# Kernel optimization log

Hardware: AMD Instinct MI355X
Metric: run time of the kernel (lower is better)

## Reference

```python
import jax, jax.numpy as jnp
import numpy as np

# ---- module hyperparameters (init_kwargs) ----
QMIN, QMAX, QBINS = -8.0, 8.0, 128
PMIN, PMAX, PBINS = -10.0, 10.0, 128
GAMMA_F = 1.0
N_TRAJ = 16384


def _grid():
    # x = arange(qmin - 4/gamma_f, qmax + 4/gamma_f + 0.1/maxp, 0.1/maxp)
    maxp = max(abs(PMIN), abs(PMAX))
    step = 0.1 / maxp
    x = np.arange(QMIN - 4.0 / GAMMA_F, QMAX + 4.0 / GAMMA_F + step, step)
    return x.astype(np.float32)


def setup_inputs() -> dict:
    key = jax.random.key(0)
    ks = jax.random.split(key, 6)
    shape = (1, N_TRAJ)
    x = jnp.asarray(_grid())
    # psi buffer: stand-in for np.interp(x, spl.x, spl.psis[-1][1]) -- a
    # localized oscillatory wavefunction sampled on the grid.
    psi = (jnp.exp(-0.5 * (x - 1.0) ** 2) * jnp.cos(2.0 * x)).astype(jnp.float32)
    return {
        "factors_re": jax.random.normal(ks[0], shape, jnp.float32),
        "factors_im": jax.random.normal(ks[1], shape, jnp.float32),
        "q_re": jax.random.normal(ks[2], shape, jnp.float32),
        "q_im": 0.5 * jax.random.normal(ks[3], shape, jnp.float32),
        "p_re": jax.random.normal(ks[4], shape, jnp.float32),
        "p_im": 0.5 * jax.random.normal(ks[5], shape, jnp.float32),
        "x": x,
        "psi": psi,
    }


def _trapz0(y, x):
    # trapezoid rule along axis 0; y: [M, N] (complex), x: [M]
    dx = jnp.diff(x)
    return jnp.sum(0.5 * (y[1:] + y[:-1]) * dx[:, None], axis=0)


def _forward(factors_re, factors_im, q_re, q_im, p_re, p_im, x, psi):
    g = GAMMA_F
    factors = factors_re + 1j * factors_im  # [1, N] complex
    # _calc_proj: xi = 2*g*q + 1j*p ; qf = Re(xi)/(2g), pf = Im(xi)
    qf = q_re - p_im / (2.0 * g)
    pf = 2.0 * g * q_im + p_re
    dq = (QMAX - QMIN) / QBINS
    dp = (PMAX - PMIN) / PBINS
    qb = jnp.floor((qf - QMIN) / dq)
    pb = jnp.floor((pf - PMIN) / dp)
    bins = (qb * PBINS + pb).astype(jnp.int32).reshape(-1)  # [N]
    n = bins.shape[0]
    # torch: enumerate(torch.unique(bins)) -> rank among sorted unique values.
    # jnp.unique inverse (size=n, large fill pads at the end) gives the same map.
    _, inv = jnp.unique(bins, return_inverse=True, size=n, fill_value=jnp.int32(2**30))
    inds = inv.reshape(qf.shape)  # [1, N] compact bin ids
    qc = (qb + 0.5) * dq + QMIN  # bin centers [1, N]
    pc = (pb + 0.5) * dp + PMIN
    # _gf: coherent-state Gaussians on grid x -> [M, N]
    norm = (2.0 * g / jnp.pi) ** 0.25
    dxq = x[:, None] - qc.reshape(-1)[None, :]  # [M, N]
    gfs = norm * jnp.exp(-g * dxq * dxq + 1j * pc.reshape(-1)[None, :] * dxq)
    gt = _trapz0(jnp.conj(gfs) * psi[:, None], x)  # [N] complex
    # _calc_pref (reconstruction): exponential prefactor that can blow up,
    # hence the nan_to_num + clamp in the original.
    pref = norm * jnp.exp(g * q_im * q_im + 1j * (p_re * q_im))  # [1, N]
    pref = (jnp.clip(jnp.nan_to_num(pref.real), -100.0, 100.0)
            + 1j * jnp.clip(jnp.nan_to_num(pref.imag), -100.0, 100.0))
    vals = pref * factors  # [1, N]
    b = vals.shape[0]
    binned = jnp.zeros_like(vals).at[jnp.arange(b)[:, None], inds].add(vals)
    loss = jnp.sum(jnp.abs(binned - gt[None, :]) ** 2)
    return jnp.sqrt(loss)


def reference(factors_re, factors_im, q_re, q_im, p_re, p_im, x, psi):
    return _forward(factors_re, factors_im, q_re, q_im, p_re, p_im, x, psi)
```

## Files before the change

### kernel.cpp

```cpp
#include <hip/hip_runtime.h>
#include <math.h>


#define PRES_WORDS 1024
#define PRES_BITS  65536
#define PRES_OFF   32768
#define CHUNKS     16
#define WINR       4.5f

__global__ void prep_kernel(const float* __restrict__ f_re, const float* __restrict__ f_im,
                            const float* __restrict__ q_re, const float* __restrict__ q_im,
                            const float* __restrict__ p_re, const float* __restrict__ p_im,
                            const float* __restrict__ x, const float* __restrict__ psi,
                            float* __restrict__ qc, float* __restrict__ pc,
                            float* __restrict__ vre, float* __restrict__ vim,
                            int* __restrict__ bins, unsigned long long* __restrict__ pres,
                            float* __restrict__ bre, float* __restrict__ bim,
                            float2* __restrict__ xw, int n, int M)
{
    int i = blockIdx.x * blockDim.x + threadIdx.x;
    if (i >= n) return;
    bre[i] = 0.0f; bim[i] = 0.0f;
    if (i < M) {
        float w;
        if (i == 0)          w = 0.5f * (x[1] - x[0]);
        else if (i == M - 1) w = 0.5f * (x[M - 1] - x[M - 2]);
        else                 w = 0.5f * (x[i + 1] - x[i - 1]);
        xw[i] = make_float2(x[i], w * psi[i] * 0.8932438417380023f);
    }
    const float norm = 0.8932438417380023f;
    float qi = q_im[i], pr = p_re[i];
    float qf = q_re[i] - 0.5f * p_im[i];
    float pf = 2.0f * qi + pr;
    float qb = floorf((qf - (-8.0f)) / 0.125f);
    float pb = floorf((pf - (-10.0f)) / 0.15625f);
    int b = (int)(qb * 128.0f + pb);
    bins[i] = b;
    int pidx = min(max(b + PRES_OFF, 0), PRES_BITS - 1);
    atomicOr(&pres[pidx >> 6], 1ull << (pidx & 63));
    qc[i] = (qb + 0.5f) * 0.125f + (-8.0f);
    pc[i] = (pb + 0.5f) * 0.15625f + (-10.0f);
    float ea = norm * expf(qi * qi);
    float s, c;
    __sincosf(pr * qi, &s, &c);
    float prr = fminf(fmaxf(ea * c, -100.0f), 100.0f);
    float pri = fminf(fmaxf(ea * s, -100.0f), 100.0f);
    float fr = f_re[i], fi = f_im[i];
    vre[i] = prr * fr - pri * fi;
    vim[i] = prr * fi + pri * fr;
}

__global__ void scatter_kernel(const int* __restrict__ bins,
                               const unsigned long long* __restrict__ pres,
                               const float* __restrict__ vre, const float* __restrict__ vim,
                               float* __restrict__ bre, float* __restrict__ bim, int n)
{
    __shared__ int lbase[PRES_WORDS];
    int tid = threadIdx.x;
    if (tid < 64) {
        int cum[16];
        int tot = 0;
        for (int k = 0; k < 16; k++) {
            cum[k] = tot;
            tot += __popcll(pres[tid * 16 + k]);
        }
        int run = tot;
        for (int off = 1; off < 64; off <<= 1) {
            int up = __shfl_up(run, off);
            if (tid >= off) run += up;
        }
        int excl = run - tot;
        for (int k = 0; k < 16; k++) lbase[tid * 16 + k] = excl + cum[k];
    }
    __syncthreads();
    int i = blockIdx.x * blockDim.x + tid;
    if (i >= n) return;
    int pidx = min(max(bins[i] + PRES_OFF, 0), PRES_BITS - 1);
    int w = pidx >> 6, bit = pidx & 63;
    unsigned long long below = pres[w] & ((bit == 0) ? 0ull : (~0ull >> (64 - bit)));
    int cid = lbase[w] + __popcll(below);
    atomicAdd(&bre[cid], vre[i]);
    atomicAdd(&bim[cid], vim[i]);
}

__global__ void gt_kernel(const float2* __restrict__ xw, const float* __restrict__ x,
                          const float* __restrict__ qc, const float* __restrict__ pc,
                          float* __restrict__ gpre, float* __restrict__ gpim,
                          int n, int M)
{
    int t = blockIdx.x * blockDim.x + threadIdx.x;
    if (t >= n) return;
    float qcn = qc[t], pcn = pc[t];
    float x0f = x[0];
    float flo = (qcn - WINR - x0f) * 100.0f;
    float fhi = (qcn + WINR - x0f) * 100.0f;
    int mlo = max(0, (int)flo - 1);
    int mhi = min(M, (int)fhi + 2);
    int len = mhi - mlo; if (len < 0) len = 0;
    int c = blockIdx.y;
    int ms = mlo + (len * c) / CHUNKS;
    int me = mlo + (len * (c + 1)) / CHUNKS;
    float sre = 0.0f, sim = 0.0f;
    for (int m = ms; m < me; m++) {
        float2 xm = xw[m];
        float dxq = xm.x - qcn;
        float e = __expf(-dxq * dxq) * xm.y;
        float s, cc;
        __sincosf(pcn * dxq, &s, &cc);
        sre = fmaf(e, cc, sre);
        sim = fmaf(-e, s, sim);
    }
    gpre[c * n + t] = sre;
    gpim[c * n + t] = sim;
}

__global__ void loss_final_kernel(const float* __restrict__ gpre, const float* __restrict__ gpim,
                                  const float* __restrict__ bre, const float* __restrict__ bim,
                                  float* __restrict__ loss, int* __restrict__ donecnt,
                                  float* __restrict__ out, int n)
{
    int t = blockIdx.x * blockDim.x + threadIdx.x;
    float v = 0.0f;
    if (t < n) {
        float sre = 0.0f, sim = 0.0f;
        for (int c = 0; c < CHUNKS; c++) {
            sre += gpre[c * n + t];
            sim += gpim[c * n + t];
        }
        float dre = bre[t] - sre;
        float dim = bim[t] - sim;
        v = dre * dre + dim * dim;
    }
#pragma unroll
    for (int off = 32; off > 0; off >>= 1) v += __shfl_down(v, off);
    __shared__ float l[4];
    int wv = threadIdx.x >> 6, ln = threadIdx.x & 63;
    if (ln == 0) l[wv] = v;
    __syncthreads();
    if (threadIdx.x == 0) {
        atomicAdd(loss, l[0] + l[1] + l[2] + l[3]);
        __threadfence();
        int old = atomicAdd(donecnt, 1);
        if (old == (int)gridDim.x - 1) {
            __threadfence();
            out[0] = sqrtf(atomicAdd(loss, 0.0f));
        }
    }
}

extern "C" void kernel_launch(void* const* d_in, const int* in_sizes, int n_in,
                              void* d_out, int out_size, void* d_ws, size_t ws_size,
                              hipStream_t stream)
{
    const float* f_re = (const float*)d_in[0];
    const float* f_im = (const float*)d_in[1];
    const float* q_re = (const float*)d_in[2];
    const float* q_im = (const float*)d_in[3];
    const float* p_re = (const float*)d_in[4];
    const float* p_im = (const float*)d_in[5];
    const float* x    = (const float*)d_in[6];
    const float* psi  = (const float*)d_in[7];
    int n = in_sizes[0];
    int M = in_sizes[6];

    float* wsf  = (float*)d_ws;
    float* qc   = wsf;
    float* pc   = qc + n;
    float* vre  = pc + n;
    float* vim  = vre + n;
    int*   bins = (int*)(vim + n);
    float* bre  = (float*)(bins + n);
    float* bim  = bre + n;
    float* gpre = bim + n;
    float* gpim = gpre + (size_t)CHUNKS * n;
    float2* xw  = (float2*)(gpim + (size_t)CHUNKS * n);
    unsigned long long* pres = (unsigned long long*)(xw + 4096);
    float* loss = (float*)(pres + PRES_WORDS);
    int*   donecnt = (int*)(loss + 1);

    hipMemsetAsync(pres, 0, PRES_WORDS * sizeof(unsigned long long) + 8, stream);

    int nb = (n + 255) / 256;
    prep_kernel<<<nb, 256, 0, stream>>>(f_re, f_im, q_re, q_im, p_re, p_im, x, psi,
                                        qc, pc, vre, vim, bins, pres, bre, bim, xw, n, M);
    scatter_kernel<<<nb, 256, 0, stream>>>(bins, pres, vre, vim, bre, bim, n);
    gt_kernel<<<dim3(nb, CHUNKS), 256, 0, stream>>>(xw, x, qc, pc, gpre, gpim, n, M);
    loss_final_kernel<<<nb, 256, 0, stream>>>(gpre, gpim, bre, bim, loss, donecnt,
                                              (float*)d_out, n);
}
```

Measured before the change: 118.1 us.

## Fuse scatter into Gaussian projection kernel and stage grid weights in shared memory

Merges the scatter-add kernel into the chunked Gaussian overlap kernel, so only the y=0 blocks perform the bin-rank computation and atomic adds. This removes one kernel launch. The grid/weight table is copied into LDS once per block instead of being read from global memory in the inner loop. The chunk count drops from 16 to 8 and the Gaussian truncation window shrinks from 4.5 to 4.0, which cuts per-thread loop work but adds slightly more tail-truncation error and assumes M fits in MCAP.

```diff
diff --git a/kernel.cpp b/kernel.cpp
--- a/kernel.cpp
+++ b/kernel.cpp
@@ -5,8 +5,9 @@
 #define PRES_WORDS 1024
 #define PRES_BITS  65536
 #define PRES_OFF   32768
-#define CHUNKS     16
-#define WINR       4.5f
+#define CHUNKS     8
+#define MCAP       2432
+#define WINR       4.0f
 
 __global__ void prep_kernel(const float* __restrict__ f_re, const float* __restrict__ f_im,
                             const float* __restrict__ q_re, const float* __restrict__ q_im,
@@ -50,20 +51,22 @@
     vim[i] = prr * fi + pri * fr;
 }
 
-__global__ void scatter_kernel(const int* __restrict__ bins,
-                               const unsigned long long* __restrict__ pres,
-                               const float* __restrict__ vre, const float* __restrict__ vim,
-                               float* __restrict__ bre, float* __restrict__ bim, int n)
+__global__ void __launch_bounds__(256) gt_scatter_kernel(
+    const float2* __restrict__ xw, const float* __restrict__ x,
+    const float* __restrict__ qc, const float* __restrict__ pc,
+    const int* __restrict__ bins, const unsigned long long* __restrict__ pres,
+    const float* __restrict__ vre, const float* __restrict__ vim,
+    float* __restrict__ bre, float* __restrict__ bim,
+    float* __restrict__ gpre, float* __restrict__ gpim, int n, int M)
 {
+    __shared__ float2 sxw[MCAP];
     __shared__ int lbase[PRES_WORDS];
     int tid = threadIdx.x;
-    if (tid < 64) {
+    for (int m = tid; m < M; m += 256) sxw[m] = xw[m];
+    if (blockIdx.y == 0 && tid < 64) {
         int cum[16];
         int tot = 0;
-        for (int k = 0; k < 16; k++) {
-            cum[k] = tot;
-            tot += __popcll(pres[tid * 16 + k]);
-        }
+        for (int k = 0; k < 16; k++) { cum[k] = tot; tot += __popcll(pres[tid * 16 + k]); }
         int run = tot;
         for (int off = 1; off < 64; off <<= 1) {
             int up = __shfl_up(run, off);
@@ -73,23 +76,16 @@
         for (int k = 0; k < 16; k++) lbase[tid * 16 + k] = excl + cum[k];
     }
     __syncthreads();
-    int i = blockIdx.x * blockDim.x + tid;
-    if (i >= n) return;
-    int pidx = min(max(bins[i] + PRES_OFF, 0), PRES_BITS - 1);
-    int w = pidx >> 6, bit = pidx & 63;
-    unsigned long long below = pres[w] & ((bit == 0) ? 0ull : (~0ull >> (64 - bit)));
-    int cid = lbase[w] + __popcll(below);
-    atomicAdd(&bre[cid], vre[i]);
-    atomicAdd(&bim[cid], vim[i]);
-}
-
-__global__ void gt_kernel(const float2* __restrict__ xw, const float* __restrict__ x,
-                          const float* __restrict__ qc, const float* __restrict__ pc,
-                          float* __restrict__ gpre, float* __restrict__ gpim,
-                          int n, int M)
-{
-    int t = blockIdx.x * blockDim.x + threadIdx.x;
+    int t = blockIdx.x * 256 + tid;
     if (t >= n) return;
+    if (blockIdx.y == 0) {
+        int pidx = min(max(bins[t] + PRES_OFF, 0), PRES_BITS - 1);
+        int w = pidx >> 6, bit = pidx & 63;
+        unsigned long long below = pres[w] & ((bit == 0) ? 0ull : (~0ull >> (64 - bit)));
+        int cid = lbase[w] + __popcll(below);
+        atomicAdd(&bre[cid], vre[t]);
+        atomicAdd(&bim[cid], vim[t]);
+    }
     float qcn = qc[t], pcn = pc[t];
     float x0f = x[0];
     float flo = (qcn - WINR - x0f) * 100.0f;
@@ -102,7 +98,7 @@
     int me = mlo + (len * (c + 1)) / CHUNKS;
     float sre = 0.0f, sim = 0.0f;
     for (int m = ms; m < me; m++) {
-        float2 xm = xw[m];
+        float2 xm = sxw[m];
         float dxq = xm.x - qcn;
         float e = __expf(-dxq * dxq) * xm.y;
         float s, cc;
@@ -174,7 +170,7 @@
     float* gpre = bim + n;
     float* gpim = gpre + (size_t)CHUNKS * n;
     float2* xw  = (float2*)(gpim + (size_t)CHUNKS * n);
-    unsigned long long* pres = (unsigned long long*)(xw + 4096);
+    unsigned long long* pres = (unsigned long long*)(xw + MCAP);
     float* loss = (float*)(pres + PRES_WORDS);
     int*   donecnt = (int*)(loss + 1);
 
@@ -183,8 +179,9 @@
     int nb = (n + 255) / 256;
     prep_kernel<<<nb, 256, 0, stream>>>(f_re, f_im, q_re, q_im, p_re, p_im, x, psi,
                                         qc, pc, vre, vim, bins, pres, bre, bim, xw, n, M);
-    scatter_kernel<<<nb, 256, 0, stream>>>(bins, pres, vre, vim, bre, bim, n);
-    gt_kernel<<<dim3(nb, CHUNKS), 256, 0, stream>>>(xw, x, qc, pc, gpre, gpim, n, M);
+    gt_scatter_kernel<<<dim3(nb, CHUNKS), 256, 0, stream>>>(xw, x, qc, pc, bins, pres,
+                                                            vre, vim, bre, bim,
+                                                            gpre, gpim, n, M);
     loss_final_kernel<<<nb, 256, 0, stream>>>(gpre, gpim, bre, bim, loss, donecnt,
                                               (float*)d_out, n);
 }
```

Result: faster. 112.6 us (-4.6%).
